# Kernel optimization log

Hardware: AMD Instinct MI355X
Metric: run time of the kernel (lower is better)

Reference implementation:

```python
import jax, jax.numpy as jnp
import numpy as np

N_P = 128          # n_particles
N_D = 3            # spatial dims (dim // n_particles)
DIM = N_P * N_D    # 384
F = 32             # n_features
H = 32             # n_hidden
B = 128            # batch
COORDS_RANGE = 5.0
EPS = 1e-6         # bgflow distances_from_vectors eps


def _edge_indices():
    # i-major ordering over all ordered pairs (i, j), i != j, matching
    # both _create_edges_indices and the off-diagonal layout of distance_vectors.
    ii, jj = np.meshgrid(np.arange(N_P), np.arange(N_P), indexing='ij')
    mask = ii != jj
    return ii[mask], jj[mask]  # each [E] with E = N_P*(N_P-1)

IDX_I, IDX_J = _edge_indices()


def setup_inputs() -> dict:
    key = jax.random.key(0)
    ks = jax.random.split(key, 12)

    def nrm(k, shape, s=0.05):
        return jax.random.normal(k, shape, jnp.float32) * s

    return dict(
        x=jax.random.normal(ks[0], (B, DIM), jnp.float32),
        h=jax.random.normal(ks[1], (B, N_P, F), jnp.float32),
        d_static=jax.random.uniform(ks[2], (B, N_P * (N_P - 1)), jnp.float32),
        # edge_network: Linear(2F+2, H), SiLU, Linear(H, F), SiLU
        e_w1=nrm(ks[3], (2 * F + 2, H)), e_b1=jnp.zeros((H,), jnp.float32),
        e_w2=nrm(ks[4], (H, F)), e_b2=jnp.zeros((F,), jnp.float32),
        # node_network: Linear(2F, H), SiLU, Linear(H, F)
        n_w1=nrm(ks[5], (2 * F, H)), n_b1=jnp.zeros((H,), jnp.float32),
        n_w2=nrm(ks[6], (H, F)), n_b2=jnp.zeros((F,), jnp.float32),
        # coord_network: Linear(F, H), SiLU, Linear(H, 1, bias=False) [xavier gain 1e-3], Tanh
        c_w1=nrm(ks[7], (F, H)), c_b1=jnp.zeros((H,), jnp.float32),
        c_w2=nrm(ks[8], (H, 1), 0.001),
        # att_mlp: Linear(F, 1), Sigmoid
        a_w=nrm(ks[9], (F, 1)), a_b=jnp.zeros((1,), jnp.float32),
    )


def reference(x, h, d_static, e_w1, e_b1, e_w2, e_b2,
              n_w1, n_b1, n_w2, n_b2, c_w1, c_b1, c_w2, a_w, a_b):
    xi = x.reshape(-1, N_P, N_D)                       # [B, n, 3]
    # distance_vectors: r_ij = x_i - x_j over ordered pairs, diagonal removed
    r = xi[:, IDX_I] - xi[:, IDX_J]                    # [B, E, 3]
    d = jnp.sqrt(jnp.sum(r * r, axis=-1) + EPS)        # [B, E]

    # edge_transformation on [h_i, h_j, d^2, d_static^2]
    hi = h[:, IDX_I]                                   # [B, E, F] gather
    hj = h[:, IDX_J]                                   # [B, E, F] gather
    ds = d_static.reshape(d.shape)
    e_in = jnp.concatenate([hi, hj, (d * d)[..., None], (ds * ds)[..., None]], axis=-1)
    m = jax.nn.silu(jax.nn.silu(e_in @ e_w1 + e_b1) @ e_w2 + e_b2)  # [B, E, F]
    m = m * jax.nn.sigmoid(m @ a_w + a_b)              # attention gate

    # coordinate update: r / (d + 1) * tanh(coord_mlp(m)), summed over neighbors
    trans = jnp.tanh(jax.nn.silu(m @ c_w1 + c_b1) @ c_w2)           # [B, E, 1]
    x_upd = (r / (d[..., None] + 1.0)) * trans                      # [B, E, 3]
    x_upd = x_upd.reshape(-1, N_P, N_P - 1, N_D).sum(axis=2)        # scatter-sum over j
    x_out = xi + x_upd * COORDS_RANGE                               # [B, n, 3]

    # node update: sum messages over neighbors, concat with h, small MLP
    m_i = m.reshape(-1, N_P, N_P - 1, F).sum(axis=2)                # [B, n, F]
    h_upd = jax.nn.silu(jnp.concatenate([h, m_i], axis=-1) @ n_w1 + n_b1) @ n_w2 + n_b2
    h_out = h + h_upd
    return x_out, h_out
```

## Files before the change

### kernel.cpp

```cpp
#include <hip/hip_runtime.h>
#include <hip/hip_bf16.h>

#define NP 128
#define NPE 127

typedef short v8s __attribute__((ext_vector_type(8)));
typedef float v4f __attribute__((ext_vector_type(4)));

#define L_NW1 0
#define L_NB1 2048
#define L_NW2 2080
#define L_NB2 3104
#define L_BUF 3136
#define L_TOT (3136 + 4 * 576)

__device__ __forceinline__ float fast_rcp(float x) { return __builtin_amdgcn_rcpf(x); }
__device__ __forceinline__ float sigmoidf_(float x) { return fast_rcp(1.0f + __expf(-x)); }
__device__ __forceinline__ float siluf(float x) { return x * sigmoidf_(x); }
__device__ __forceinline__ float tanhf_fast(float x) {
    return 1.0f - 2.0f * fast_rcp(1.0f + __expf(2.0f * x));
}
__device__ __forceinline__ short f2bf(float x) {
    __hip_bfloat16 h = __float2bfloat16(x);
    return *reinterpret_cast<short*>(&h);
}

__global__ __launch_bounds__(128)
void hc_kernel(const float* __restrict__ Hin, const float* __restrict__ EW1,
               const float* __restrict__ EB1, float* __restrict__ HC)
{
    __shared__ float sw[64 * 32 + 32];
    const int t = threadIdx.x;
    for (int idx = t; idx < 64 * 32; idx += 128) sw[idx] = EW1[idx];
    if (t < 32) sw[2048 + t] = EB1[t];
    __syncthreads();

    const int row = blockIdx.x * 128 + t;
    const float* hp = &Hin[row * 32];
    float h[32];
    #pragma unroll
    for (int g = 0; g < 8; ++g) {
        const float4 v = *(const float4*)&hp[g * 4];
        h[g*4+0] = v.x; h[g*4+1] = v.y; h[g*4+2] = v.z; h[g*4+3] = v.w;
    }
    float a1[32], a2[32];
    #pragma unroll
    for (int o = 0; o < 32; ++o) { a1[o] = sw[2048 + o]; a2[o] = 0.f; }
    #pragma unroll
    for (int k = 0; k < 32; ++k) {
        const float a = h[k];
        #pragma unroll
        for (int o = 0; o < 32; ++o) {
            a1[o] = fmaf(a, sw[k * 32 + o], a1[o]);
            a2[o] = fmaf(a, sw[(32 + k) * 32 + o], a2[o]);
        }
    }
    float* op = &HC[row * 64];
    #pragma unroll
    for (int o = 0; o < 32; ++o) { op[o] = a1[o]; op[32 + o] = a2[o]; }
}

__global__ __launch_bounds__(256)
void eq_gnn_main(const float* __restrict__ X, const float* __restrict__ Hin,
                 const float* __restrict__ DS, const float* __restrict__ HC,
                 const float* __restrict__ EW1, const float* __restrict__ EW2,
                 const float* __restrict__ EB2,
                 const float* __restrict__ NW1, const float* __restrict__ NB1,
                 const float* __restrict__ NW2, const float* __restrict__ NB2,
                 const float* __restrict__ CW1, const float* __restrict__ CB1,
                 const float* __restrict__ CW2,
                 const float* __restrict__ AW,  const float* __restrict__ AB,
                 float* __restrict__ OUT)
{
    __shared__ float sw[L_TOT];
    const int tid = threadIdx.x;

    for (int idx = tid; idx < 2048; idx += 256) sw[L_NW1 + idx] = NW1[idx];
    for (int idx = tid; idx < 1024; idx += 256) sw[L_NW2 + idx] = NW2[idx];
    if (tid < 32) { sw[L_NB1 + tid] = NB1[tid]; sw[L_NB2 + tid] = NB2[tid]; }
    __syncthreads();

    const int lane = tid & 63;
    const int wid  = tid >> 6;
    const int node = blockIdx.x * 4 + wid;
    const int b = node >> 7, i = node & 127;
    const int m16 = lane & 15;
    const int q   = lane >> 4;

    float* buf = &sw[L_BUF + wid * 576];

    v8s Bw2[2], Bc1[2];
    #pragma unroll
    for (int t = 0; t < 2; ++t)
        #pragma unroll
        for (int j = 0; j < 8; ++j) {
            Bw2[t][j] = f2bf(EW2[(q * 8 + j) * 32 + m16 + 16 * t]);
            Bc1[t][j] = f2bf(CW1[(q * 8 + j) * 32 + m16 + 16 * t]);
        }
    float w64c[8], w65c[8], awc[8], cw2c[8], hcic[8];
    #pragma unroll
    for (int j = 0; j < 8; ++j) {
        w64c[j] = EW1[64 * 32 + q * 8 + j];
        w65c[j] = EW1[65 * 32 + q * 8 + j];
        awc[j]  = AW[q * 8 + j];
        cw2c[j] = CW2[q * 8 + j];
        hcic[j] = HC[node * 64 + q * 8 + j];
    }
    const float b2a  = EB2[m16], b2b  = EB2[m16 + 16];
    const float cb1a = CB1[m16], cb1b = CB1[m16 + 16];
    const float ab0  = AB[0];
    const float xi0 = X[b * 384 + i * 3 + 0];
    const float xi1 = X[b * 384 + i * 3 + 1];
    const float xi2 = X[b * 384 + i * 3 + 2];

    float ms[8];
    #pragma unroll
    for (int j = 0; j < 8; ++j) ms[j] = 0.f;
    float xc0 = 0.f, xc1 = 0.f, xc2 = 0.f;

    #pragma unroll 1
    for (int tl = 0; tl < 8; ++tl) {
        const int e = tl * 16 + m16;
        const float valid = (e < NPE) ? 1.f : 0.f;
        const int js = (e < NPE) ? e : 126;
        const int j = js + ((js >= i) ? 1 : 0);

        const float* xj = &X[b * 384 + j * 3];
        const float r0 = xi0 - xj[0], r1 = xi1 - xj[1], r2 = xi2 - xj[2];
        const float d2 = fmaf(r0, r0, fmaf(r1, r1, fmaf(r2, r2, 1e-6f)));
        const float d  = sqrtf(d2);
        const float dsv = DS[b * 16256 + i * 127 + js];
        const float ds2 = dsv * dsv;

        const float* hcj = &HC[(b * 128 + j) * 64 + 32 + q * 8];
        const float4 hj0 = *(const float4*)&hcj[0];
        const float4 hj1 = *(const float4*)&hcj[4];
        float hjv[8] = {hj0.x, hj0.y, hj0.z, hj0.w, hj1.x, hj1.y, hj1.z, hj1.w};
        v8s A;
        #pragma unroll
        for (int jj = 0; jj < 8; ++jj) {
            float v = hcic[jj] + hjv[jj];
            v = fmaf(d2, w64c[jj], v);
            v = fmaf(ds2, w65c[jj], v);
            A[jj] = f2bf(siluf(v));
        }

        v4f c0 = {b2a, b2a, b2a, b2a};
        v4f c1 = {b2b, b2b, b2b, b2b};
        c0 = __builtin_amdgcn_mfma_f32_16x16x32_bf16(A, Bw2[0], c0, 0, 0, 0);
        c1 = __builtin_amdgcn_mfma_f32_16x16x32_bf16(A, Bw2[1], c1, 0, 0, 0);

        #pragma unroll
        for (int r = 0; r < 4; ++r) {
            buf[(q * 4 + r) * 36 + m16]      = siluf(c0[r]);
            buf[(q * 4 + r) * 36 + m16 + 16] = siluf(c1[r]);
        }
        const float4 mlo = *(const float4*)&buf[m16 * 36 + q * 8];
        const float4 mhi = *(const float4*)&buf[m16 * 36 + q * 8 + 4];
        float mA[8] = {mlo.x, mlo.y, mlo.z, mlo.w, mhi.x, mhi.y, mhi.z, mhi.w};

        float lg = 0.f;
        #pragma unroll
        for (int jj = 0; jj < 8; ++jj) lg = fmaf(mA[jj], awc[jj], lg);
        lg += __shfl_xor(lg, 16, 64);
        lg += __shfl_xor(lg, 32, 64);
        const float att = sigmoidf_(lg + ab0) * valid;
        v8s Ag;
        #pragma unroll
        for (int jj = 0; jj < 8; ++jj) {
            const float g = mA[jj] * att;
            ms[jj] += g;
            Ag[jj] = f2bf(g);
        }

        v4f e0 = {cb1a, cb1a, cb1a, cb1a};
        v4f e1 = {cb1b, cb1b, cb1b, cb1b};
        e0 = __builtin_amdgcn_mfma_f32_16x16x32_bf16(Ag, Bc1[0], e0, 0, 0, 0);
        e1 = __builtin_amdgcn_mfma_f32_16x16x32_bf16(Ag, Bc1[1], e1, 0, 0, 0);
        #pragma unroll
        for (int r = 0; r < 4; ++r) {
            buf[(q * 4 + r) * 36 + m16]      = siluf(e0[r]);
            buf[(q * 4 + r) * 36 + m16 + 16] = siluf(e1[r]);
        }
        const float4 clo = *(const float4*)&buf[m16 * 36 + q * 8];
        const float4 chi = *(const float4*)&buf[m16 * 36 + q * 8 + 4];
        float tr = clo.x * cw2c[0] + clo.y * cw2c[1] + clo.z * cw2c[2] + clo.w * cw2c[3]
                 + chi.x * cw2c[4] + chi.y * cw2c[5] + chi.z * cw2c[6] + chi.w * cw2c[7];
        tr += __shfl_xor(tr, 16, 64);
        tr += __shfl_xor(tr, 32, 64);
        const float coef = tanhf_fast(tr) * fast_rcp(d + 1.0f) * valid;

        xc0 = fmaf(r0, coef, xc0);
        xc1 = fmaf(r1, coef, xc1);
        xc2 = fmaf(r2, coef, xc2);
    }

    #pragma unroll
    for (int jj = 0; jj < 8; ++jj) {
        float v = ms[jj];
        v += __shfl_xor(v, 1, 64); v += __shfl_xor(v, 2, 64);
        v += __shfl_xor(v, 4, 64); v += __shfl_xor(v, 8, 64);
        ms[jj] = v;
    }
    {
        float v0 = xc0, v1 = xc1, v2 = xc2;
        #pragma unroll
        for (int s = 1; s < 64; s <<= 1) {
            v0 += __shfl_xor(v0, s, 64);
            v1 += __shfl_xor(v1, s, 64);
            v2 += __shfl_xor(v2, s, 64);
        }
        xc0 = v0 * 0.25f; xc1 = v1 * 0.25f; xc2 = v2 * 0.25f;
    }

    if (lane < 3) {
        const float xiv = (lane == 0) ? xi0 : ((lane == 1) ? xi1 : xi2);
        const float xcv = (lane == 0) ? xc0 : ((lane == 1) ? xc1 : xc2);
        OUT[b * 384 + i * 3 + lane] = fmaf(xcv, 5.0f, xiv);
    }

    if (m16 == 0) {
        #pragma unroll
        for (int jj = 0; jj < 8; ++jj) buf[q * 8 + jj] = ms[jj];
    }
    const int o = lane & 31;
    float a1 = sw[L_NB1 + o];
    #pragma unroll
    for (int k = 0; k < 32; ++k)
        a1 = fmaf(Hin[node * 32 + k], sw[L_NW1 + k * 32 + o], a1);
    #pragma unroll
    for (int k = 0; k < 32; ++k)
        a1 = fmaf(buf[k], sw[L_NW1 + (32 + k) * 32 + o], a1);
    const float s1 = siluf(a1);
    float a2 = sw[L_NB2 + o];
    #pragma unroll
    for (int k = 0; k < 32; ++k)
        a2 = fmaf(__shfl(s1, k, 64), sw[L_NW2 + k * 32 + o], a2);
    if (lane < 32)
        OUT[49152 + node * 32 + o] = Hin[node * 32 + o] + a2;
}

extern "C" void kernel_launch(void* const* d_in, const int* in_sizes, int n_in,
                              void* d_out, int out_size, void* d_ws, size_t ws_size,
                              hipStream_t stream) {
    (void)in_sizes; (void)n_in; (void)out_size; (void)ws_size;
    float* HC = (float*)d_ws;

    hc_kernel<<<dim3(128), dim3(128), 0, stream>>>(
        (const float*)d_in[1], (const float*)d_in[3], (const float*)d_in[4], HC);

    eq_gnn_main<<<dim3(4096), dim3(256), 0, stream>>>(
        (const float*)d_in[0],  (const float*)d_in[1],  (const float*)d_in[2], HC,
        (const float*)d_in[3],  (const float*)d_in[5],  (const float*)d_in[6],
        (const float*)d_in[7],  (const float*)d_in[8],  (const float*)d_in[9],  (const float*)d_in[10],
        (const float*)d_in[11], (const float*)d_in[12], (const float*)d_in[13],
        (const float*)d_in[14], (const float*)d_in[15],
        (float*)d_out);
}
```

Before: 197.6 us.

## Fuse per-node projection into main kernel and transpose MFMA operands to drop LDS round-trips

Removes the separate hc_kernel launch. Each block now recomputes the h_j projection for all 128 nodes of its batch element with MFMA into shared memory, and computes h_i·W1 plus the per-edge geometry (r, 1/(d+1), d², ds²) into shared memory up front. The edge MLP MFMAs are transposed, with weights as the A operand and activations as B, so outputs land per lane in the layout needed for the next stage. This drops the LDS write/readback between MFMAs. In exchange, the h_j projection is redundantly recomputed by 32 blocks per batch element, the h_j projection now runs in bf16, and the node MLP reads weights from global memory instead of LDS.

```diff
diff --git a/kernel.cpp b/kernel.cpp
--- a/kernel.cpp
+++ b/kernel.cpp
@@ -7,196 +7,192 @@
 typedef short v8s __attribute__((ext_vector_type(8)));
 typedef float v4f __attribute__((ext_vector_type(4)));
 
-#define L_NW1 0
-#define L_NB1 2048
-#define L_NW2 2080
-#define L_NB2 3104
-#define L_BUF 3136
-#define L_TOT (3136 + 4 * 576)
-
-__device__ __forceinline__ float fast_rcp(float x) { return __builtin_amdgcn_rcpf(x); }
-__device__ __forceinline__ float sigmoidf_(float x) { return fast_rcp(1.0f + __expf(-x)); }
-__device__ __forceinline__ float siluf(float x) { return x * sigmoidf_(x); }
-__device__ __forceinline__ float tanhf_fast(float x) {
+#define L_HCJ  0
+#define L_GEOM 4608
+#define L_HCI  8704
+#define L_TOT  8832
+
+__device__ __forceinline__ float fast_rcp(float x){ return __builtin_amdgcn_rcpf(x); }
+__device__ __forceinline__ float sigmoidf_(float x){ return fast_rcp(1.0f + __expf(-x)); }
+__device__ __forceinline__ float siluf(float x){ return x * sigmoidf_(x); }
+__device__ __forceinline__ float tanhf_fast(float x){
     return 1.0f - 2.0f * fast_rcp(1.0f + __expf(2.0f * x));
 }
-__device__ __forceinline__ short f2bf(float x) {
+__device__ __forceinline__ short f2bf(float x){
     __hip_bfloat16 h = __float2bfloat16(x);
     return *reinterpret_cast<short*>(&h);
 }
 
-__global__ __launch_bounds__(128)
-void hc_kernel(const float* __restrict__ Hin, const float* __restrict__ EW1,
-               const float* __restrict__ EB1, float* __restrict__ HC)
+__global__ __launch_bounds__(256)
+void eq_gnn_fused(const float* __restrict__ X, const float* __restrict__ Hin,
+                  const float* __restrict__ DS,
+                  const float* __restrict__ EW1, const float* __restrict__ EB1,
+                  const float* __restrict__ EW2, const float* __restrict__ EB2,
+                  const float* __restrict__ NW1, const float* __restrict__ NB1,
+                  const float* __restrict__ NW2, const float* __restrict__ NB2,
+                  const float* __restrict__ CW1, const float* __restrict__ CB1,
+                  const float* __restrict__ CW2,
+                  const float* __restrict__ AW,  const float* __restrict__ AB,
+                  float* __restrict__ OUT)
 {
-    __shared__ float sw[64 * 32 + 32];
-    const int t = threadIdx.x;
-    for (int idx = t; idx < 64 * 32; idx += 128) sw[idx] = EW1[idx];
-    if (t < 32) sw[2048 + t] = EB1[t];
-    __syncthreads();
-
-    const int row = blockIdx.x * 128 + t;
-    const float* hp = &Hin[row * 32];
-    float h[32];
-    #pragma unroll
-    for (int g = 0; g < 8; ++g) {
-        const float4 v = *(const float4*)&hp[g * 4];
-        h[g*4+0] = v.x; h[g*4+1] = v.y; h[g*4+2] = v.z; h[g*4+3] = v.w;
-    }
-    float a1[32], a2[32];
-    #pragma unroll
-    for (int o = 0; o < 32; ++o) { a1[o] = sw[2048 + o]; a2[o] = 0.f; }
-    #pragma unroll
-    for (int k = 0; k < 32; ++k) {
-        const float a = h[k];
-        #pragma unroll
-        for (int o = 0; o < 32; ++o) {
-            a1[o] = fmaf(a, sw[k * 32 + o], a1[o]);
-            a2[o] = fmaf(a, sw[(32 + k) * 32 + o], a2[o]);
-        }
-    }
-    float* op = &HC[row * 64];
-    #pragma unroll
-    for (int o = 0; o < 32; ++o) { op[o] = a1[o]; op[32 + o] = a2[o]; }
-}
-
-__global__ __launch_bounds__(256)
-void eq_gnn_main(const float* __restrict__ X, const float* __restrict__ Hin,
-                 const float* __restrict__ DS, const float* __restrict__ HC,
-                 const float* __restrict__ EW1, const float* __restrict__ EW2,
-                 const float* __restrict__ EB2,
-                 const float* __restrict__ NW1, const float* __restrict__ NB1,
-                 const float* __restrict__ NW2, const float* __restrict__ NB2,
-                 const float* __restrict__ CW1, const float* __restrict__ CB1,
-                 const float* __restrict__ CW2,
-                 const float* __restrict__ AW,  const float* __restrict__ AB,
-                 float* __restrict__ OUT)
-{
-    __shared__ float sw[L_TOT];
-    const int tid = threadIdx.x;
-
-    for (int idx = tid; idx < 2048; idx += 256) sw[L_NW1 + idx] = NW1[idx];
-    for (int idx = tid; idx < 1024; idx += 256) sw[L_NW2 + idx] = NW2[idx];
-    if (tid < 32) { sw[L_NB1 + tid] = NB1[tid]; sw[L_NB2 + tid] = NB2[tid]; }
-    __syncthreads();
-
+    __shared__ float sm[L_TOT];
+    const int tid  = threadIdx.x;
     const int lane = tid & 63;
     const int wid  = tid >> 6;
-    const int node = blockIdx.x * 4 + wid;
-    const int b = node >> 7, i = node & 127;
-    const int m16 = lane & 15;
-    const int q   = lane >> 4;
-
-    float* buf = &sw[L_BUF + wid * 576];
-
-    v8s Bw2[2], Bc1[2];
-    #pragma unroll
-    for (int t = 0; t < 2; ++t)
-        #pragma unroll
-        for (int j = 0; j < 8; ++j) {
-            Bw2[t][j] = f2bf(EW2[(q * 8 + j) * 32 + m16 + 16 * t]);
-            Bc1[t][j] = f2bf(CW1[(q * 8 + j) * 32 + m16 + 16 * t]);
-        }
-    float w64c[8], w65c[8], awc[8], cw2c[8], hcic[8];
-    #pragma unroll
-    for (int j = 0; j < 8; ++j) {
-        w64c[j] = EW1[64 * 32 + q * 8 + j];
-        w65c[j] = EW1[65 * 32 + q * 8 + j];
-        awc[j]  = AW[q * 8 + j];
-        cw2c[j] = CW2[q * 8 + j];
-        hcic[j] = HC[node * 64 + q * 8 + j];
-    }
-    const float b2a  = EB2[m16], b2b  = EB2[m16 + 16];
-    const float cb1a = CB1[m16], cb1b = CB1[m16 + 16];
-    const float ab0  = AB[0];
-    const float xi0 = X[b * 384 + i * 3 + 0];
-    const float xi1 = X[b * 384 + i * 3 + 1];
-    const float xi2 = X[b * 384 + i * 3 + 2];
+    const int m16  = lane & 15;
+    const int q    = lane >> 4;
+    const int bI   = blockIdx.x >> 5;
+    const int grp  = blockIdx.x & 31;
+    const int i    = grp * 4 + wid;
+    const int node = bI * 128 + i;
+
+    {
+        v8s Aj0, Aj1;
+        #pragma unroll
+        for (int jj = 0; jj < 8; ++jj){
+            Aj0[jj] = f2bf(EW1[(32 + q*8 + jj) * 32 + m16]);
+            Aj1[jj] = f2bf(EW1[(32 + q*8 + jj) * 32 + 16 + m16]);
+        }
+        #pragma unroll
+        for (int rr = 0; rr < 2; ++rr){
+            const int row = (wid * 2 + rr) * 16 + m16;
+            const float* hp = &Hin[(bI * 128 + row) * 32 + q * 8];
+            const float4 h0 = *(const float4*)&hp[0];
+            const float4 h1 = *(const float4*)&hp[4];
+            v8s Bh;
+            Bh[0]=f2bf(h0.x); Bh[1]=f2bf(h0.y); Bh[2]=f2bf(h0.z); Bh[3]=f2bf(h0.w);
+            Bh[4]=f2bf(h1.x); Bh[5]=f2bf(h1.y); Bh[6]=f2bf(h1.z); Bh[7]=f2bf(h1.w);
+            v4f d0 = {0.f,0.f,0.f,0.f}, d1 = {0.f,0.f,0.f,0.f};
+            d0 = __builtin_amdgcn_mfma_f32_16x16x32_bf16(Aj0, Bh, d0, 0, 0, 0);
+            d1 = __builtin_amdgcn_mfma_f32_16x16x32_bf16(Aj1, Bh, d1, 0, 0, 0);
+            #pragma unroll
+            for (int r = 0; r < 4; ++r){
+                sm[L_HCJ + row * 36 + q*4 + r]      = d0[r];
+                sm[L_HCJ + row * 36 + 16 + q*4 + r] = d1[r];
+            }
+        }
+    }
+    if (tid < 128){
+        const int nl = tid >> 5, o = tid & 31;
+        const float* hp = &Hin[(bI * 128 + grp * 4 + nl) * 32];
+        float acc = EB1[o];
+        #pragma unroll
+        for (int k = 0; k < 32; ++k) acc = fmaf(hp[k], EW1[k * 32 + o], acc);
+        sm[L_HCI + nl * 32 + o] = acc;
+    }
+    float* sg = &sm[L_GEOM + wid * 1024];
+    const float xi0 = X[bI*384 + i*3 + 0];
+    const float xi1 = X[bI*384 + i*3 + 1];
+    const float xi2 = X[bI*384 + i*3 + 2];
+    #pragma unroll
+    for (int p = 0; p < 2; ++p){
+        const int slot = lane + 64 * p;
+        const int js = (slot < NPE) ? slot : 126;
+        const int j = js + ((js >= i) ? 1 : 0);
+        const float* xj = &X[bI*384 + j*3];
+        const float r0 = xi0 - xj[0], r1 = xi1 - xj[1], r2 = xi2 - xj[2];
+        const float d2 = fmaf(r0, r0, fmaf(r1, r1, fmaf(r2, r2, 1e-6f)));
+        const float d  = sqrtf(d2);
+        const float rinv = fast_rcp(d + 1.0f);
+        const float dsv = DS[bI*16256 + i*127 + js];
+        *(float4*)&sg[slot*8]     = make_float4(r0, r1, r2, rinv);
+        *(float2*)&sg[slot*8 + 4] = make_float2(d2, dsv * dsv);
+    }
+    __syncthreads();
+
+    v8s Aw20, Aw21, Ac0, Ac1;
+    #pragma unroll
+    for (int jj = 0; jj < 8; ++jj){
+        Aw20[jj] = f2bf(EW2[(q*8 + jj) * 32 + m16]);
+        Aw21[jj] = f2bf(EW2[(q*8 + jj) * 32 + 16 + m16]);
+        const int tau = (jj < 4) ? (q*4 + jj) : (16 + q*4 + (jj - 4));
+        Ac0[jj] = f2bf(CW1[tau * 32 + m16]);
+        Ac1[jj] = f2bf(CW1[tau * 32 + 16 + m16]);
+    }
+    const float4 w64a = *(const float4*)&EW1[64*32 + q*8];
+    const float4 w64b = *(const float4*)&EW1[64*32 + q*8 + 4];
+    const float4 w65a = *(const float4*)&EW1[65*32 + q*8];
+    const float4 w65b = *(const float4*)&EW1[65*32 + q*8 + 4];
+    const float4 b2A = *(const float4*)&EB2[q*4];
+    const float4 b2B = *(const float4*)&EB2[16 + q*4];
+    const float4 cbA = *(const float4*)&CB1[q*4];
+    const float4 cbB = *(const float4*)&CB1[16 + q*4];
+    const float4 cwA = *(const float4*)&CW2[q*4];
+    const float4 cwB = *(const float4*)&CW2[16 + q*4];
+    const float4 awA = *(const float4*)&AW[q*4];
+    const float4 awB = *(const float4*)&AW[16 + q*4];
+    const float ab0 = AB[0];
+    const float4 hci0 = *(const float4*)&sm[L_HCI + wid*32 + q*8];
+    const float4 hci1 = *(const float4*)&sm[L_HCI + wid*32 + q*8 + 4];
 
     float ms[8];
     #pragma unroll
-    for (int j = 0; j < 8; ++j) ms[j] = 0.f;
+    for (int jj = 0; jj < 8; ++jj) ms[jj] = 0.f;
     float xc0 = 0.f, xc1 = 0.f, xc2 = 0.f;
 
     #pragma unroll 1
-    for (int tl = 0; tl < 8; ++tl) {
+    for (int tl = 0; tl < 8; ++tl){
         const int e = tl * 16 + m16;
         const float valid = (e < NPE) ? 1.f : 0.f;
         const int js = (e < NPE) ? e : 126;
         const int j = js + ((js >= i) ? 1 : 0);
 
-        const float* xj = &X[b * 384 + j * 3];
-        const float r0 = xi0 - xj[0], r1 = xi1 - xj[1], r2 = xi2 - xj[2];
-        const float d2 = fmaf(r0, r0, fmaf(r1, r1, fmaf(r2, r2, 1e-6f)));
-        const float d  = sqrtf(d2);
-        const float dsv = DS[b * 16256 + i * 127 + js];
-        const float ds2 = dsv * dsv;
-
-        const float* hcj = &HC[(b * 128 + j) * 64 + 32 + q * 8];
-        const float4 hj0 = *(const float4*)&hcj[0];
-        const float4 hj1 = *(const float4*)&hcj[4];
-        float hjv[8] = {hj0.x, hj0.y, hj0.z, hj0.w, hj1.x, hj1.y, hj1.z, hj1.w};
-        v8s A;
-        #pragma unroll
-        for (int jj = 0; jj < 8; ++jj) {
-            float v = hcic[jj] + hjv[jj];
-            v = fmaf(d2, w64c[jj], v);
-            v = fmaf(ds2, w65c[jj], v);
-            A[jj] = f2bf(siluf(v));
-        }
-
-        v4f c0 = {b2a, b2a, b2a, b2a};
-        v4f c1 = {b2b, b2b, b2b, b2b};
-        c0 = __builtin_amdgcn_mfma_f32_16x16x32_bf16(A, Bw2[0], c0, 0, 0, 0);
-        c1 = __builtin_amdgcn_mfma_f32_16x16x32_bf16(A, Bw2[1], c1, 0, 0, 0);
-
-        #pragma unroll
-        for (int r = 0; r < 4; ++r) {
-            buf[(q * 4 + r) * 36 + m16]      = siluf(c0[r]);
-            buf[(q * 4 + r) * 36 + m16 + 16] = siluf(c1[r]);
-        }
-        const float4 mlo = *(const float4*)&buf[m16 * 36 + q * 8];
-        const float4 mhi = *(const float4*)&buf[m16 * 36 + q * 8 + 4];
-        float mA[8] = {mlo.x, mlo.y, mlo.z, mlo.w, mhi.x, mhi.y, mhi.z, mhi.w};
-
-        float lg = 0.f;
-        #pragma unroll
-        for (int jj = 0; jj < 8; ++jj) lg = fmaf(mA[jj], awc[jj], lg);
+        const float2 dd = *(const float2*)&sg[e*8 + 4];
+        const float4 hj0 = *(const float4*)&sm[L_HCJ + j*36 + q*8];
+        const float4 hj1 = *(const float4*)&sm[L_HCJ + j*36 + q*8 + 4];
+
+        v8s Bt;
+        Bt[0] = f2bf(siluf(fmaf(dd.x, w64a.x, fmaf(dd.y, w65a.x, hci0.x + hj0.x))));
+        Bt[1] = f2bf(siluf(fmaf(dd.x, w64a.y, fmaf(dd.y, w65a.y, hci0.y + hj0.y))));
+        Bt[2] = f2bf(siluf(fmaf(dd.x, w64a.z, fmaf(dd.y, w65a.z, hci0.z + hj0.z))));
+        Bt[3] = f2bf(siluf(fmaf(dd.x, w64a.w, fmaf(dd.y, w65a.w, hci0.w + hj0.w))));
+        Bt[4] = f2bf(siluf(fmaf(dd.x, w64b.x, fmaf(dd.y, w65b.x, hci1.x + hj1.x))));
+        Bt[5] = f2bf(siluf(fmaf(dd.x, w64b.y, fmaf(dd.y, w65b.y, hci1.y + hj1.y))));
+        Bt[6] = f2bf(siluf(fmaf(dd.x, w64b.z, fmaf(dd.y, w65b.z, hci1.z + hj1.z))));
+        Bt[7] = f2bf(siluf(fmaf(dd.x, w64b.w, fmaf(dd.y, w65b.w, hci1.w + hj1.w))));
+
+        v4f c0 = {b2A.x, b2A.y, b2A.z, b2A.w};
+        v4f c1 = {b2B.x, b2B.y, b2B.z, b2B.w};
+        c0 = __builtin_amdgcn_mfma_f32_16x16x32_bf16(Aw20, Bt, c0, 0, 0, 0);
+        c1 = __builtin_amdgcn_mfma_f32_16x16x32_bf16(Aw21, Bt, c1, 0, 0, 0);
+        const float s0 = siluf(c0[0]), s1 = siluf(c0[1]), s2 = siluf(c0[2]), s3 = siluf(c0[3]);
+        const float s4 = siluf(c1[0]), s5 = siluf(c1[1]), s6 = siluf(c1[2]), s7 = siluf(c1[3]);
+
+        float lg = s0*awA.x + s1*awA.y + s2*awA.z + s3*awA.w
+                 + s4*awB.x + s5*awB.y + s6*awB.z + s7*awB.w;
         lg += __shfl_xor(lg, 16, 64);
         lg += __shfl_xor(lg, 32, 64);
         const float att = sigmoidf_(lg + ab0) * valid;
-        v8s Ag;
-        #pragma unroll
-        for (int jj = 0; jj < 8; ++jj) {
-            const float g = mA[jj] * att;
-            ms[jj] += g;
-            Ag[jj] = f2bf(g);
-        }
-
-        v4f e0 = {cb1a, cb1a, cb1a, cb1a};
-        v4f e1 = {cb1b, cb1b, cb1b, cb1b};
-        e0 = __builtin_amdgcn_mfma_f32_16x16x32_bf16(Ag, Bc1[0], e0, 0, 0, 0);
-        e1 = __builtin_amdgcn_mfma_f32_16x16x32_bf16(Ag, Bc1[1], e1, 0, 0, 0);
-        #pragma unroll
-        for (int r = 0; r < 4; ++r) {
-            buf[(q * 4 + r) * 36 + m16]      = siluf(e0[r]);
-            buf[(q * 4 + r) * 36 + m16 + 16] = siluf(e1[r]);
-        }
-        const float4 clo = *(const float4*)&buf[m16 * 36 + q * 8];
-        const float4 chi = *(const float4*)&buf[m16 * 36 + q * 8 + 4];
-        float tr = clo.x * cw2c[0] + clo.y * cw2c[1] + clo.z * cw2c[2] + clo.w * cw2c[3]
-                 + chi.x * cw2c[4] + chi.y * cw2c[5] + chi.z * cw2c[6] + chi.w * cw2c[7];
+
+        v8s Bm;
+        float g;
+        g = s0*att; ms[0] += g; Bm[0] = f2bf(g);
+        g = s1*att; ms[1] += g; Bm[1] = f2bf(g);
+        g = s2*att; ms[2] += g; Bm[2] = f2bf(g);
+        g = s3*att; ms[3] += g; Bm[3] = f2bf(g);
+        g = s4*att; ms[4] += g; Bm[4] = f2bf(g);
+        g = s5*att; ms[5] += g; Bm[5] = f2bf(g);
+        g = s6*att; ms[6] += g; Bm[6] = f2bf(g);
+        g = s7*att; ms[7] += g; Bm[7] = f2bf(g);
+
+        v4f e0 = {cbA.x, cbA.y, cbA.z, cbA.w};
+        v4f e1 = {cbB.x, cbB.y, cbB.z, cbB.w};
+        e0 = __builtin_amdgcn_mfma_f32_16x16x32_bf16(Ac0, Bm, e0, 0, 0, 0);
+        e1 = __builtin_amdgcn_mfma_f32_16x16x32_bf16(Ac1, Bm, e1, 0, 0, 0);
+        float tr = siluf(e0[0])*cwA.x + siluf(e0[1])*cwA.y + siluf(e0[2])*cwA.z + siluf(e0[3])*cwA.w
+                 + siluf(e1[0])*cwB.x + siluf(e1[1])*cwB.y + siluf(e1[2])*cwB.z + siluf(e1[3])*cwB.w;
         tr += __shfl_xor(tr, 16, 64);
         tr += __shfl_xor(tr, 32, 64);
-        const float coef = tanhf_fast(tr) * fast_rcp(d + 1.0f) * valid;
-
-        xc0 = fmaf(r0, coef, xc0);
-        xc1 = fmaf(r1, coef, xc1);
-        xc2 = fmaf(r2, coef, xc2);
-    }
-
-    #pragma unroll
-    for (int jj = 0; jj < 8; ++jj) {
+
+        const float4 rv = *(const float4*)&sg[e*8];
+        const float coef = tanhf_fast(tr) * rv.w * valid;
+        xc0 = fmaf(rv.x, coef, xc0);
+        xc1 = fmaf(rv.y, coef, xc1);
+        xc2 = fmaf(rv.z, coef, xc2);
+    }
+
+    #pragma unroll
+    for (int jj = 0; jj < 8; ++jj){
         float v = ms[jj];
         v += __shfl_xor(v, 1, 64); v += __shfl_xor(v, 2, 64);
         v += __shfl_xor(v, 4, 64); v += __shfl_xor(v, 8, 64);
@@ -205,7 +201,7 @@
     {
         float v0 = xc0, v1 = xc1, v2 = xc2;
         #pragma unroll
-        for (int s = 1; s < 64; s <<= 1) {
+        for (int s = 1; s < 64; s <<= 1){
             v0 += __shfl_xor(v0, s, 64);
             v1 += __shfl_xor(v1, s, 64);
             v2 += __shfl_xor(v2, s, 64);
@@ -213,45 +209,42 @@
         xc0 = v0 * 0.25f; xc1 = v1 * 0.25f; xc2 = v2 * 0.25f;
     }
 
-    if (lane < 3) {
+    if (lane < 3){
         const float xiv = (lane == 0) ? xi0 : ((lane == 1) ? xi1 : xi2);
         const float xcv = (lane == 0) ? xc0 : ((lane == 1) ? xc1 : xc2);
-        OUT[b * 384 + i * 3 + lane] = fmaf(xcv, 5.0f, xiv);
-    }
-
-    if (m16 == 0) {
-        #pragma unroll
-        for (int jj = 0; jj < 8; ++jj) buf[q * 8 + jj] = ms[jj];
-    }
+        OUT[bI*384 + i*3 + lane] = fmaf(xcv, 5.0f, xiv);
+    }
+
+    if (m16 == 0){
+        #pragma unroll
+        for (int jj = 0; jj < 8; ++jj){
+            const int tau = (jj < 4) ? (q*4 + jj) : (16 + q*4 + (jj - 4));
+            sg[tau] = ms[jj];
+        }
+    }
+
     const int o = lane & 31;
-    float a1 = sw[L_NB1 + o];
-    #pragma unroll
-    for (int k = 0; k < 32; ++k)
-        a1 = fmaf(Hin[node * 32 + k], sw[L_NW1 + k * 32 + o], a1);
-    #pragma unroll
-    for (int k = 0; k < 32; ++k)
-        a1 = fmaf(buf[k], sw[L_NW1 + (32 + k) * 32 + o], a1);
-    const float s1 = siluf(a1);
-    float a2 = sw[L_NB2 + o];
-    #pragma unroll
-    for (int k = 0; k < 32; ++k)
-        a2 = fmaf(__shfl(s1, k, 64), sw[L_NW2 + k * 32 + o], a2);
+    const float* hp = &Hin[node * 32];
+    float a1 = NB1[o];
+    #pragma unroll
+    for (int k = 0; k < 32; ++k) a1 = fmaf(hp[k], NW1[k * 32 + o], a1);
+    #pragma unroll
+    for (int k = 0; k < 32; ++k) a1 = fmaf(sg[k], NW1[(32 + k) * 32 + o], a1);
+    const float s1v = siluf(a1);
+    float a2 = NB2[o];
+    #pragma unroll
+    for (int k = 0; k < 32; ++k) a2 = fmaf(__shfl(s1v, k, 64), NW2[k * 32 + o], a2);
     if (lane < 32)
-        OUT[49152 + node * 32 + o] = Hin[node * 32 + o] + a2;
+        OUT[49152 + node * 32 + o] = hp[o] + a2;
 }
 
 extern "C" void kernel_launch(void* const* d_in, const int* in_sizes, int n_in,
                               void* d_out, int out_size, void* d_ws, size_t ws_size,
                               hipStream_t stream) {
-    (void)in_sizes; (void)n_in; (void)out_size; (void)ws_size;
-    float* HC = (float*)d_ws;
-
-    hc_kernel<<<dim3(128), dim3(128), 0, stream>>>(
-        (const float*)d_in[1], (const float*)d_in[3], (const float*)d_in[4], HC);
-
-    eq_gnn_main<<<dim3(4096), dim3(256), 0, stream>>>(
-        (const float*)d_in[0],  (const float*)d_in[1],  (const float*)d_in[2], HC,
-        (const float*)d_in[3],  (const float*)d_in[5],  (const float*)d_in[6],
+    (void)in_sizes; (void)n_in; (void)out_size; (void)d_ws; (void)ws_size;
+    eq_gnn_fused<<<dim3(4096), dim3(256), 0, stream>>>(
+        (const float*)d_in[0],  (const float*)d_in[1],  (const float*)d_in[2],
+        (const float*)d_in[3],  (const float*)d_in[4],  (const float*)d_in[5],  (const float*)d_in[6],
         (const float*)d_in[7],  (const float*)d_in[8],  (const float*)d_in[9],  (const float*)d_in[10],
         (const float*)d_in[11], (const float*)d_in[12], (const float*)d_in[13],
         (const float*)d_in[14], (const float*)d_in[15],
```

Measured after the change: 171.0 us. 1.16x faster.
